# Kernel tuning notes

Measured on AMD Instinct MI355X. Metric: run time of the kernel, lower is better.

## Reference

```python
import jax, jax.numpy as jnp
import numpy as np

N = 50000   # nodes
E = 400000  # edges
R = 35      # num_relations
B = 12      # num_bases
C = 128     # hidden_conv_dim (heads=1)
T = 4       # node types: load, gen, load_gen, ext
HL = 38     # hidden_lin_dim
OUT = 2


def setup_inputs() -> dict:
    key = jax.random.key(0)
    ks = jax.random.split(key, 24)
    s = 0.1  # param scale
    inp = {
        'x': jax.random.normal(ks[0], (N, 2), jnp.float32),
        'edge_index': jax.random.randint(ks[1], (2, E), 0, N, jnp.int32),
        'edge_type': jax.random.randint(ks[2], (E,), 0, R, jnp.int32),
        'edge_attr': jax.random.normal(ks[3], (E, 2), jnp.float32),
        'node_type': jax.random.randint(ks[4], (N,), 0, T, jnp.int32),
        'basis': jax.random.normal(ks[5], (B, 2, C), jnp.float32) * s,
        'att_rel': jax.random.normal(ks[6], (R, B), jnp.float32) * s,
        'q_att': jax.random.normal(ks[7], (C, 1), jnp.float32) * s,
        'k_att': jax.random.normal(ks[8], (C, 1), jnp.float32) * s,
        'e_att': jax.random.normal(ks[9], (C, 1), jnp.float32) * s,
        'lin_edge_W': jax.random.normal(ks[10], (2, C), jnp.float32) * s,
        'conv_bias': jax.random.normal(ks[11], (C,), jnp.float32) * s,
        'lin0_W': jax.random.normal(ks[12], (T, C, HL), jnp.float32) * s,
        'lin0_b': jax.random.normal(ks[13], (T, HL), jnp.float32) * s,
        'lin1_W': jax.random.normal(ks[14], (T, HL, HL), jnp.float32) * s,
        'lin1_b': jax.random.normal(ks[15], (T, HL), jnp.float32) * s,
        'lin2_W': jax.random.normal(ks[16], (T, HL, HL), jnp.float32) * s,
        'lin2_b': jax.random.normal(ks[17], (T, HL), jnp.float32) * s,
        'fin_W': jax.random.normal(ks[18], (T, HL, OUT), jnp.float32) * s,
        'fin_b': jax.random.normal(ks[19], (T, OUT), jnp.float32) * s,
    }
    return inp


def _segment_softmax(alpha, dst, n):
    # PyG softmax: max is detached, eps=1e-16 on the denominator
    amax = jax.lax.stop_gradient(jax.ops.segment_max(alpha, dst, num_segments=n))
    ex = jnp.exp(alpha - amax[dst])
    den = jax.ops.segment_sum(ex, dst, num_segments=n) + 1e-16
    return ex / den[dst]


def _per_type_linear(xv, W, b, t):
    # apply node-type-specific Linear: [N,d] x [T,d,h] -> pick row type
    y = jnp.einsum('nd,tdh->nth', xv, W)              # [N,T,h]
    y = jnp.take_along_axis(y, t[:, None, None], axis=1)[:, 0]
    return y + b[t]


def reference(x, edge_index, edge_type, edge_attr, node_type,
              basis, att_rel, q_att, k_att, e_att, lin_edge_W, conv_bias,
              lin0_W, lin0_b, lin1_W, lin1_b, lin2_W, lin2_b, fin_W, fin_b):
    n = x.shape[0]
    src, dst = edge_index[0], edge_index[1]
    # RGATConv with basis decomposition: per-relation weight [R, in=2, C]
    w = jnp.einsum('rb,bio->rio', att_rel, basis)
    w_e = w[edge_type]                                 # [E,2,C] edge gather
    out_i = jnp.einsum('ei,eic->ec', x[dst], w_e)      # [E,C]
    out_j = jnp.einsum('ei,eic->ec', x[src], w_e)      # [E,C]
    ke = (edge_attr @ lin_edge_W) @ e_att              # [E,1]
    alpha = out_i @ q_att + out_j @ k_att + ke         # additive self-attention
    alpha = jax.nn.leaky_relu(alpha, 0.2)
    alpha = _segment_softmax(alpha, dst, n)            # across-relation segment softmax
    msg = alpha * out_j                                # heads=1 -> [E,C]
    agg = jax.ops.segment_sum(msg, dst, num_segments=n) + conv_bias
    h = jax.nn.leaky_relu(agg, 0.2)                    # forward activation (dropout: eval)
    t = node_type
    h = _per_type_linear(jax.nn.relu(h), lin0_W, lin0_b, t)
    h = _per_type_linear(jax.nn.relu(h), lin1_W, lin1_b, t)
    h = _per_type_linear(jax.nn.relu(h), lin2_W, lin2_b, t)
    out = _per_type_linear(h, fin_W, fin_b, t)         # [N,2]
    # load nodes (type 0): second output passes through abs
    load_out = jnp.concatenate([out[:, :1], jnp.abs(out[:, 1:2])], axis=1)
    return jnp.where((t == 0)[:, None], load_out, out)
```

## Files before the change

kernel.cpp:

```cpp
#include <hip/hip_runtime.h>
#include <math.h>

#define N_NODES 50000
#define N_EDGES 400000
#define R_REL   35
#define B_BASES 12
#define C_DIM   128
#define HL_DIM  38
#define RI2     70
#define NP      50304
#define NB_HIST 196
#define NBUCK   786
#define EPB     2048
#define CAP     704

#define OFF_WT     0
#define OFF_WQ     8960
#define OFF_WK     9030
#define OFF_LE     9100
#define OFF_META   9104
#define OFF_HBLK   9120
#define OFF_BBASE  9904
#define OFF_PERM   10688
#define OFF_INV    60688
#define OFF_ECUR   110992
#define OFF_EREC   111780

#define CH    0
#define ST    3584
#define HH    0
#define Y0T   0
#define W1S   3264
#define W2S   4784
#define Y1T   6304
#define Y2T   0
#define W0Q   8344
#define SM_DINV 9624
#define SM_FW   9688
#define SM_FB   9764
#define LDS_FLOATS 9766

__global__ __launch_bounds__(256) void k_init(const int* __restrict__ node_type,
                                              const float* __restrict__ basis,
                                              const float* __restrict__ att_rel,
                                              float* __restrict__ ws) {
    int b = blockIdx.x, tid = threadIdx.x;
    if (b < NB_HIST) {
        __shared__ int lh[4];
        if (tid < 4) lh[tid] = 0;
        __syncthreads();
        int i = b * 256 + tid;
        if (i < N_NODES) atomicAdd(&lh[node_type[i]], 1);
        __syncthreads();
        if (tid < 4) ((int*)(ws + OFF_HBLK))[b * 4 + tid] = lh[tid];
    } else if (b < NB_HIST + 35) {
        int idx = (b - NB_HIST) * 256 + tid;
        if (idx < RI2 * C_DIM) {
            int c  = idx & (C_DIM - 1);
            int ri = idx >> 7;
            int r = ri >> 1, ii = ri & 1;
            float acc = 0.f;
            #pragma unroll
            for (int bb = 0; bb < B_BASES; ++bb)
                acc += att_rel[r * B_BASES + bb] * basis[(bb * 2 + ii) * C_DIM + c];
            ws[OFF_WT + idx] = acc;
        }
    } else {
        for (int i = tid; i < NBUCK; i += 256) ((int*)(ws + OFF_ECUR))[i] = 0;
    }
}

__global__ __launch_bounds__(256) void k_scanproj(const float* __restrict__ q_att,
                                                  const float* __restrict__ k_att,
                                                  const float* __restrict__ e_att,
                                                  const float* __restrict__ lin_edge_W,
                                                  float* __restrict__ ws) {
    int b = blockIdx.x, tid = threadIdx.x;
    int lane = tid & 63, wv = tid >> 6;
    if (b == 0) {
        __shared__ int lh[NB_HIST * 4];
        __shared__ int basel[4];
        const int* hblk = (const int*)(ws + OFF_HBLK);
        for (int i = tid; i < NB_HIST * 4; i += 256) lh[i] = hblk[i];
        __syncthreads();
        __shared__ int tot[4];
        if (tid < 4) {
            int run = 0;
            for (int bb = 0; bb < NB_HIST; ++bb) {
                int v = lh[bb * 4 + tid];
                lh[bb * 4 + tid] = run;
                run += v;
            }
            tot[tid] = run;
        }
        __syncthreads();
        if (tid == 0) {
            int* meta = (int*)(ws + OFF_META);
            int t0 = tot[0], t1 = tot[1], t2 = tot[2], t3 = tot[3];
            int b1 = ((t0 + 63) >> 6) << 6;
            int b2 = b1 + (((t1 + 63) >> 6) << 6);
            int b3 = b2 + (((t2 + 63) >> 6) << 6);
            meta[0] = t0; meta[1] = t1; meta[2] = t2; meta[3] = t3;
            meta[4] = 0;  meta[5] = b1; meta[6] = b2; meta[7] = b3;
            basel[0] = 0; basel[1] = b1; basel[2] = b2; basel[3] = b3;
        }
        __syncthreads();
        for (int i = tid; i < NB_HIST * 4; i += 256)
            ((int*)(ws + OFF_BBASE))[i] = basel[i & 3] + lh[i];
    } else {
        int u = (b - 1) * 4 + wv;
        if (u < RI2) {
            const float* wr = ws + OFF_WT + u * C_DIM;
            float w1 = wr[lane], w2 = wr[64 + lane];
            float aq = w1 * q_att[lane] + w2 * q_att[64 + lane];
            float ak = w1 * k_att[lane] + w2 * k_att[64 + lane];
            #pragma unroll
            for (int off = 32; off; off >>= 1) {
                aq += __shfl_xor(aq, off, 64);
                ak += __shfl_xor(ak, off, 64);
            }
            if (lane == 0) { ws[OFF_WQ + u] = aq; ws[OFF_WK + u] = ak; }
        } else if (u < 72) {
            int j = u - RI2;
            const float* er = lin_edge_W + j * C_DIM;
            float a = er[lane] * e_att[lane] + er[64 + lane] * e_att[64 + lane];
            #pragma unroll
            for (int off = 32; off; off >>= 1) a += __shfl_xor(a, off, 64);
            if (lane == 0) ws[OFF_LE + j] = a;
        }
    }
}

__global__ __launch_bounds__(256) void k_perm(const int* __restrict__ node_type,
                                              float* __restrict__ ws) {
    __shared__ int wcnt[4][4];
    int tid = threadIdx.x;
    int lane = tid & 63, wv = tid >> 6;
    int n = blockIdx.x * 256 + tid;
    bool active = n < N_NODES;
    int ty = active ? node_type[n] : -1;
    int myrank = 0;
    #pragma unroll
    for (int t = 0; t < 4; ++t) {
        unsigned long long m = __ballot(ty == t);
        if (lane == 0) wcnt[wv][t] = __popcll(m);
        if (ty == t) myrank = __popcll(m & ((1ULL << lane) - 1ULL));
    }
    __syncthreads();
    if (active) {
        int pre = 0;
        for (int w2 = 0; w2 < wv; ++w2) pre += wcnt[w2][ty];
        int p = ((const int*)(ws + OFF_BBASE))[blockIdx.x * 4 + ty] + pre + myrank;
        ((int*)(ws + OFF_PERM))[n] = p;
        ((int*)(ws + OFF_INV))[p] = n;
    }
}

__global__ __launch_bounds__(256) void k_escatter(const float* __restrict__ x,
                                                  const int* __restrict__ edge_index,
                                                  const int* __restrict__ edge_type,
                                                  const float* __restrict__ edge_attr,
                                                  float* __restrict__ ws) {
    __shared__ int hist[NBUCK];
    __shared__ int sbase[NBUCK];
    __shared__ float swq[RI2], swk[RI2], sle[2];
    int tid = threadIdx.x;
    for (int i = tid; i < NBUCK; i += 256) hist[i] = 0;
    if (tid < RI2) { swq[tid] = ws[OFF_WQ + tid]; swk[tid] = ws[OFF_WK + tid]; }
    if (tid < 2) sle[tid] = ws[OFF_LE + tid];
    __syncthreads();

    const int* perm = (const int*)(ws + OFF_PERM);
    int base = blockIdx.x * EPB;
    int   rb[8], rm[8];
    float rex[8], rsx[8], rsy[8];
    #pragma unroll
    for (int k = 0; k < 8; ++k) {
        int e = base + k * 256 + tid;
        rb[k] = -1;
        if (e < N_EDGES) {
            int src = edge_index[e];
            int dst = edge_index[N_EDGES + e];
            int r   = edge_type[e];
            int p   = perm[dst];
            float2 ea = *(const float2*)(edge_attr + 2 * e);
            float2 xs = *(const float2*)(x + 2 * src);
            float2 xd = *(const float2*)(x + 2 * dst);
            float alpha = xd.x * swq[2 * r] + xd.y * swq[2 * r + 1]
                        + xs.x * swk[2 * r] + xs.y * swk[2 * r + 1]
                        + ea.x * sle[0]     + ea.y * sle[1];
            alpha = alpha > 0.f ? alpha : 0.2f * alpha;
            float ex = __expf(alpha);
            rb[k]  = p >> 6;
            rm[k]  = (r << 6) | (p & 63);
            rex[k] = ex;
            rsx[k] = ex * xs.x;
            rsy[k] = ex * xs.y;
            atomicAdd(&hist[rb[k]], 1);
        }
    }
    __syncthreads();
    int* gcur = (int*)(ws + OFF_ECUR);
    for (int i = tid; i < NBUCK; i += 256) {
        int c = hist[i];
        sbase[i] = (c > 0) ? atomicAdd(&gcur[i], c) : 0;
    }
    __syncthreads();
    float4* rec = (float4*)(ws + OFF_EREC);
    #pragma unroll
    for (int k = 0; k < 8; ++k) {
        if (rb[k] >= 0) {
            int slot = atomicAdd(&sbase[rb[k]], 1);
            rec[(size_t)rb[k] * CAP + slot] =
                make_float4(__int_as_float(rm[k]), rex[k], rsx[k], rsy[k]);
        }
    }
}

__global__ __launch_bounds__(256) void k_node(
        const float* __restrict__ ws, const float* __restrict__ conv_bias,
        const float* __restrict__ lin0_W, const float* __restrict__ lin0_b,
        const float* __restrict__ lin1_W, const float* __restrict__ lin1_b,
        const float* __restrict__ lin2_W, const float* __restrict__ lin2_b,
        const float* __restrict__ fin_W,  const float* __restrict__ fin_b,
        float* __restrict__ out) {
    __shared__ float L[LDS_FLOATS];
    int tid  = threadIdx.x;
    int lane = tid & 63;
    int wv   = tid >> 6;
    int p0   = blockIdx.x * 64;

    const int* meta = (const int*)(ws + OFF_META);
    int b1 = meta[5], b2 = meta[6], b3 = meta[7];
    int t  = (p0 >= b1) + (p0 >= b2) + (p0 >= b3);
    int bp = meta[4 + t];
    int cnt = meta[t];

    for (int i = tid; i < RI2 * 68; i += 256) L[ST + i] = 0.f;
    if (tid < 64) L[SM_DINV + tid] = 0.f;
    if (tid >= 64 && tid < 142) {
        int i = tid - 64;
        if (i < 76) L[SM_FW + i] = fin_W[t * 76 + i];
        else        L[SM_FB + i - 76] = fin_b[t * 2 + i - 76];
    }
    const float* wT_g = ws + OFF_WT;
    for (int i4 = tid; i4 < 448; i4 += 256) {
        float4 v = ((const float4*)wT_g)[i4];
        *(float4*)&L[CH + i4 * 4] = v;
    }
    __syncthreads();

    {
        int ecnt = ((const int*)(ws + OFF_ECUR))[blockIdx.x];
        const float4* rec = (const float4*)(ws + OFF_EREC) + (size_t)blockIdx.x * CAP;
        for (int i = tid; i < ecnt; i += 256) {
            float4 v = rec[i];
            int m = __float_as_int(v.x);
            int n = m & 63, r = m >> 6;
            atomicAdd(&L[ST + (2 * r) * 68 + n],     v.z);
            atomicAdd(&L[ST + (2 * r + 1) * 68 + n], v.w);
            atomicAdd(&L[SM_DINV + n],               v.y);
        }
    }
    __syncthreads();
    if (tid < 64) L[SM_DINV + tid] = 1.0f / (L[SM_DINV + tid] + 1e-16f);

    int ng = lane & 15, cg_ = lane >> 4;
    int c0 = wv * 32 + cg_ * 8;
    float acc[32];
    #pragma unroll
    for (int i = 0; i < 32; ++i) acc[i] = 0.f;
    int cur = 0;
    for (int q = 0; q < 5; ++q) {
        float4 pf0, pf1;
        if (q < 4) {
            const float4* src = (const float4*)(wT_g + (q + 1) * 1792);
            pf0 = src[tid];
            if (tid < 192) pf1 = src[tid + 256];
        }
        const float* wb = &L[CH + cur * 1792];
        #pragma unroll
        for (int kk = 0; kk < 14; ++kk) {
            float4 a4 = *(const float4*)&L[ST + (q * 14 + kk) * 68 + ng * 4];
            float4 wa = *(const float4*)&wb[kk * 128 + c0];
            float4 wc = *(const float4*)&wb[kk * 128 + c0 + 4];
            float a_[4] = {a4.x, a4.y, a4.z, a4.w};
            float w_[8] = {wa.x, wa.y, wa.z, wa.w, wc.x, wc.y, wc.z, wc.w};
            #pragma unroll
            for (int ni = 0; ni < 4; ++ni)
                #pragma unroll
                for (int ci = 0; ci < 8; ++ci)
                    acc[ni * 8 + ci] += a_[ni] * w_[ci];
        }
        if (q < 4) {
            float* dstb = &L[CH + (cur ^ 1) * 1792];
            *(float4*)&dstb[tid * 4] = pf0;
            if (tid < 192) *(float4*)&dstb[(tid + 256) * 4] = pf1;
        }
        cur ^= 1;
        __syncthreads();
    }

    {
        float4 dv = *(const float4*)&L[SM_DINV + ng * 4];
        float d_[4] = {dv.x, dv.y, dv.z, dv.w};
        #pragma unroll
        for (int ci = 0; ci < 8; ++ci) {
            float cb = conv_bias[c0 + ci];
            float4 hv;
            float h0 = acc[0 * 8 + ci] * d_[0] + cb;
            float h1 = acc[1 * 8 + ci] * d_[1] + cb;
            float h2 = acc[2 * 8 + ci] * d_[2] + cb;
            float h3 = acc[3 * 8 + ci] * d_[3] + cb;
            hv.x = h0 > 0.f ? h0 : 0.f;
            hv.y = h1 > 0.f ? h1 : 0.f;
            hv.z = h2 > 0.f ? h2 : 0.f;
            hv.w = h3 > 0.f ? h3 : 0.f;
            *(float4*)&L[HH + (c0 + ci) * 64 + ng * 4] = hv;
        }
    }
    __syncthreads();

    const float* W0g = lin0_W + t * C_DIM * HL_DIM;
    int jg = lane >> 4;
    int j0 = wv * 16 + jg * 4;
    float acc2[16];
    #pragma unroll
    for (int i = 0; i < 16; ++i) acc2[i] = 0.f;
    for (int q = 0; q < 4; ++q) {
        for (int i = tid; i < 1216; i += 256) {
            int cc = i / 38, j = i - cc * 38;
            L[W0Q + cc * 40 + j] = W0g[q * 1216 + i];
        }
        __syncthreads();
        if (wv < 3) {
            #pragma unroll 4
            for (int kk = 0; kk < 32; ++kk) {
                int c = q * 32 + kk;
                float4 a4 = *(const float4*)&L[HH + c * 64 + ng * 4];
                float4 w4 = *(const float4*)&L[W0Q + kk * 40 + j0];
                float a_[4] = {a4.x, a4.y, a4.z, a4.w};
                float w_[4] = {w4.x, w4.y, w4.z, w4.w};
                #pragma unroll
                for (int ni = 0; ni < 4; ++ni)
                    #pragma unroll
                    for (int ji = 0; ji < 4; ++ji)
                        acc2[ni * 4 + ji] += a_[ni] * w_[ji];
            }
        }
        __syncthreads();
    }
    if (wv < 3) {
        #pragma unroll
        for (int ji = 0; ji < 4; ++ji) {
            int j = j0 + ji;
            float b = (j < HL_DIM) ? lin0_b[t * HL_DIM + j] : 0.f;
            float4 yv;
            float y0 = acc2[0 * 4 + ji] + b;
            float y1 = acc2[1 * 4 + ji] + b;
            float y2 = acc2[2 * 4 + ji] + b;
            float y3 = acc2[3 * 4 + ji] + b;
            yv.x = y0 > 0.f ? y0 : 0.f;
            yv.y = y1 > 0.f ? y1 : 0.f;
            yv.z = y2 > 0.f ? y2 : 0.f;
            yv.w = y3 > 0.f ? y3 : 0.f;
            *(float4*)&L[Y0T + j * 68 + ng * 4] = yv;
        }
    }
    {
        const float* W1g = lin1_W + t * HL_DIM * HL_DIM;
        const float* W2g = lin2_W + t * HL_DIM * HL_DIM;
        for (int i = tid; i < 1444; i += 256) {
            int cc = i / 38, j = i - cc * 38;
            L[W1S + cc * 40 + j] = W1g[i];
            L[W2S + cc * 40 + j] = W2g[i];
        }
    }
    __syncthreads();

    float acc3[16];
    #pragma unroll
    for (int i = 0; i < 16; ++i) acc3[i] = 0.f;
    if (wv < 3) {
        #pragma unroll 2
        for (int kk = 0; kk < HL_DIM; ++kk) {
            float4 a4 = *(const float4*)&L[Y0T + kk * 68 + ng * 4];
            float4 w4 = *(const float4*)&L[W1S + kk * 40 + j0];
            float a_[4] = {a4.x, a4.y, a4.z, a4.w};
            float w_[4] = {w4.x, w4.y, w4.z, w4.w};
            #pragma unroll
            for (int ni = 0; ni < 4; ++ni)
                #pragma unroll
                for (int ji = 0; ji < 4; ++ji)
                    acc3[ni * 4 + ji] += a_[ni] * w_[ji];
        }
        #pragma unroll
        for (int ji = 0; ji < 4; ++ji) {
            int j = j0 + ji;
            float b = (j < HL_DIM) ? lin1_b[t * HL_DIM + j] : 0.f;
            float4 yv;
            float y0 = acc3[0 * 4 + ji] + b;
            float y1 = acc3[1 * 4 + ji] + b;
            float y2 = acc3[2 * 4 + ji] + b;
            float y3 = acc3[3 * 4 + ji] + b;
            yv.x = y0 > 0.f ? y0 : 0.f;
            yv.y = y1 > 0.f ? y1 : 0.f;
            yv.z = y2 > 0.f ? y2 : 0.f;
            yv.w = y3 > 0.f ? y3 : 0.f;
            *(float4*)&L[Y1T + j * 68 + ng * 4] = yv;
        }
    }
    __syncthreads();

    if (wv < 3) {
        float acc4[16];
        #pragma unroll
        for (int i = 0; i < 16; ++i) acc4[i] = 0.f;
        #pragma unroll 2
        for (int kk = 0; kk < HL_DIM; ++kk) {
            float4 a4 = *(const float4*)&L[Y1T + kk * 68 + ng * 4];
            float4 w4 = *(const float4*)&L[W2S + kk * 40 + j0];
            float a_[4] = {a4.x, a4.y, a4.z, a4.w};
            float w_[4] = {w4.x, w4.y, w4.z, w4.w};
            #pragma unroll
            for (int ni = 0; ni < 4; ++ni)
                #pragma unroll
                for (int ji = 0; ji < 4; ++ji)
                    acc4[ni * 4 + ji] += a_[ni] * w_[ji];
        }
        #pragma unroll
        for (int ji = 0; ji < 4; ++ji) {
            int j = j0 + ji;
            float b = (j < HL_DIM) ? lin2_b[t * HL_DIM + j] : 0.f;
            float4 yv;
            yv.x = acc4[0 * 4 + ji] + b;
            yv.y = acc4[1 * 4 + ji] + b;
            yv.z = acc4[2 * 4 + ji] + b;
            yv.w = acc4[3 * 4 + ji] + b;
            *(float4*)&L[Y2T + j * 68 + ng * 4] = yv;
        }
    }
    __syncthreads();

    if (tid < 64) {
        int p = p0 + tid;
        bool valid = (p - bp) < cnt;
        float o0 = L[SM_FB], o1 = L[SM_FB + 1];
        for (int jj = 0; jj < HL_DIM; ++jj) {
            float v = L[Y2T + jj * 68 + tid];
            float2 f = *(const float2*)&L[SM_FW + jj * 2];
            o0 += v * f.x;
            o1 += v * f.y;
        }
        if (t == 0) o1 = fabsf(o1);
        if (valid) {
            int orig = ((const int*)(ws + OFF_INV))[p];
            ((float2*)out)[orig] = make_float2(o0, o1);
        }
    }
}

extern "C" void kernel_launch(void* const* d_in, const int* in_sizes, int n_in,
                              void* d_out, int out_size, void* d_ws, size_t ws_size,
                              hipStream_t stream) {
    const float* x          = (const float*)d_in[0];
    const int*   edge_index = (const int*)  d_in[1];
    const int*   edge_type  = (const int*)  d_in[2];
    const float* edge_attr  = (const float*)d_in[3];
    const int*   node_type  = (const int*)  d_in[4];
    const float* basis      = (const float*)d_in[5];
    const float* att_rel    = (const float*)d_in[6];
    const float* q_att      = (const float*)d_in[7];
    const float* k_att      = (const float*)d_in[8];
    const float* e_att      = (const float*)d_in[9];
    const float* lin_edge_W = (const float*)d_in[10];
    const float* conv_bias  = (const float*)d_in[11];
    const float* lin0_W     = (const float*)d_in[12];
    const float* lin0_b     = (const float*)d_in[13];
    const float* lin1_W     = (const float*)d_in[14];
    const float* lin1_b     = (const float*)d_in[15];
    const float* lin2_W     = (const float*)d_in[16];
    const float* lin2_b     = (const float*)d_in[17];
    const float* fin_W      = (const float*)d_in[18];
    const float* fin_b      = (const float*)d_in[19];

    float* ws  = (float*)d_ws;
    float* out = (float*)d_out;

    k_init    <<<NB_HIST + 35 + 1, 256, 0, stream>>>(node_type, basis, att_rel, ws);
    k_scanproj<<<19, 256, 0, stream>>>(q_att, k_att, e_att, lin_edge_W, ws);
    k_perm    <<<NB_HIST, 256, 0, stream>>>(node_type, ws);
    k_escatter<<<NB_HIST, 256, 0, stream>>>(x, edge_index, edge_type, edge_attr, ws);
    k_node    <<<NBUCK, 256, 0, stream>>>(ws, conv_bias,
                                          lin0_W, lin0_b, lin1_W, lin1_b,
                                          lin2_W, lin2_b, fin_W, fin_b, out);
}
```

Before: 177.7 us.

## Fold scan/projection kernel into init and perm kernels to drop a launch

Removes the k_scanproj kernel. The q/k/e attention projections move into extra k_init blocks, which recompute the basis-combined weights directly instead of reading them back from the workspace. Each k_perm block now redundantly scans the per-block type histogram to find its own prefix and the type bases. This removes one kernel launch and its dependency gap, at the cost of redundant serial scan work in every perm block.

```diff
diff --git a/kernel.cpp b/kernel.cpp
--- a/kernel.cpp
+++ b/kernel.cpp
@@ -20,7 +20,6 @@
 #define OFF_LE     9100
 #define OFF_META   9104
 #define OFF_HBLK   9120
-#define OFF_BBASE  9904
 #define OFF_PERM   10688
 #define OFF_INV    60688
 #define OFF_ECUR   110992
@@ -43,6 +42,10 @@
 __global__ __launch_bounds__(256) void k_init(const int* __restrict__ node_type,
                                               const float* __restrict__ basis,
                                               const float* __restrict__ att_rel,
+                                              const float* __restrict__ q_att,
+                                              const float* __restrict__ k_att,
+                                              const float* __restrict__ e_att,
+                                              const float* __restrict__ lin_edge_W,
                                               float* __restrict__ ws) {
     int b = blockIdx.x, tid = threadIdx.x;
     if (b < NB_HIST) {
@@ -65,77 +68,72 @@
                 acc += att_rel[r * B_BASES + bb] * basis[(bb * 2 + ii) * C_DIM + c];
             ws[OFF_WT + idx] = acc;
         }
+    } else if (b == NB_HIST + 35) {
+        for (int i = tid; i < NBUCK; i += 256) ((int*)(ws + OFF_ECUR))[i] = 0;
     } else {
-        for (int i = tid; i < NBUCK; i += 256) ((int*)(ws + OFF_ECUR))[i] = 0;
-    }
-}
-
-__global__ __launch_bounds__(256) void k_scanproj(const float* __restrict__ q_att,
-                                                  const float* __restrict__ k_att,
-                                                  const float* __restrict__ e_att,
-                                                  const float* __restrict__ lin_edge_W,
-                                                  float* __restrict__ ws) {
-    int b = blockIdx.x, tid = threadIdx.x;
-    int lane = tid & 63, wv = tid >> 6;
-    if (b == 0) {
-        __shared__ int lh[NB_HIST * 4];
-        __shared__ int basel[4];
-        const int* hblk = (const int*)(ws + OFF_HBLK);
-        for (int i = tid; i < NB_HIST * 4; i += 256) lh[i] = hblk[i];
-        __syncthreads();
-        __shared__ int tot[4];
-        if (tid < 4) {
-            int run = 0;
-            for (int bb = 0; bb < NB_HIST; ++bb) {
-                int v = lh[bb * 4 + tid];
-                lh[bb * 4 + tid] = run;
-                run += v;
+        int lane = tid & 63, wv = tid >> 6;
+        int u = (b - (NB_HIST + 36)) * 4 + wv;
+        if (u < 2 * RI2) {
+            int ri = (u < RI2) ? u : (u - RI2);
+            int r = ri >> 1, ii = ri & 1;
+            const float* av = att_rel + r * B_BASES;
+            const float* bs = basis + ii * C_DIM;
+            float w1 = 0.f, w2 = 0.f;
+            #pragma unroll
+            for (int bb = 0; bb < B_BASES; ++bb) {
+                float a = av[bb];
+                w1 += a * bs[bb * 2 * C_DIM + lane];
+                w2 += a * bs[bb * 2 * C_DIM + 64 + lane];
             }
-            tot[tid] = run;
-        }
-        __syncthreads();
-        if (tid == 0) {
-            int* meta = (int*)(ws + OFF_META);
-            int t0 = tot[0], t1 = tot[1], t2 = tot[2], t3 = tot[3];
-            int b1 = ((t0 + 63) >> 6) << 6;
-            int b2 = b1 + (((t1 + 63) >> 6) << 6);
-            int b3 = b2 + (((t2 + 63) >> 6) << 6);
-            meta[0] = t0; meta[1] = t1; meta[2] = t2; meta[3] = t3;
-            meta[4] = 0;  meta[5] = b1; meta[6] = b2; meta[7] = b3;
-            basel[0] = 0; basel[1] = b1; basel[2] = b2; basel[3] = b3;
-        }
-        __syncthreads();
-        for (int i = tid; i < NB_HIST * 4; i += 256)
-            ((int*)(ws + OFF_BBASE))[i] = basel[i & 3] + lh[i];
-    } else {
-        int u = (b - 1) * 4 + wv;
-        if (u < RI2) {
-            const float* wr = ws + OFF_WT + u * C_DIM;
-            float w1 = wr[lane], w2 = wr[64 + lane];
-            float aq = w1 * q_att[lane] + w2 * q_att[64 + lane];
-            float ak = w1 * k_att[lane] + w2 * k_att[64 + lane];
-            #pragma unroll
-            for (int off = 32; off; off >>= 1) {
-                aq += __shfl_xor(aq, off, 64);
-                ak += __shfl_xor(ak, off, 64);
-            }
-            if (lane == 0) { ws[OFF_WQ + u] = aq; ws[OFF_WK + u] = ak; }
-        } else if (u < 72) {
-            int j = u - RI2;
+            const float* qk = (u < RI2) ? q_att : k_att;
+            float s = w1 * qk[lane] + w2 * qk[64 + lane];
+            #pragma unroll
+            for (int off = 32; off; off >>= 1) s += __shfl_xor(s, off, 64);
+            if (lane == 0) ws[((u < RI2) ? OFF_WQ : OFF_WK) + ri] = s;
+        } else if (u < 2 * RI2 + 2) {
+            int j = u - 2 * RI2;
             const float* er = lin_edge_W + j * C_DIM;
-            float a = er[lane] * e_att[lane] + er[64 + lane] * e_att[64 + lane];
-            #pragma unroll
-            for (int off = 32; off; off >>= 1) a += __shfl_xor(a, off, 64);
-            if (lane == 0) ws[OFF_LE + j] = a;
+            float s = er[lane] * e_att[lane] + er[64 + lane] * e_att[64 + lane];
+            #pragma unroll
+            for (int off = 32; off; off >>= 1) s += __shfl_xor(s, off, 64);
+            if (lane == 0) ws[OFF_LE + j] = s;
         }
     }
 }
 
 __global__ __launch_bounds__(256) void k_perm(const int* __restrict__ node_type,
                                               float* __restrict__ ws) {
+    __shared__ int lh[NB_HIST * 4];
+    __shared__ int pre[4], tot[4], basel[4];
     __shared__ int wcnt[4][4];
     int tid = threadIdx.x;
     int lane = tid & 63, wv = tid >> 6;
+    const int* hblk = (const int*)(ws + OFF_HBLK);
+    for (int i = tid; i < NB_HIST * 4; i += 256) lh[i] = hblk[i];
+    __syncthreads();
+    if (tid < 4) {
+        int run = 0, mypre = 0;
+        for (int bb = 0; bb < NB_HIST; ++bb) {
+            if (bb == (int)blockIdx.x) mypre = run;
+            run += lh[bb * 4 + tid];
+        }
+        pre[tid] = mypre;
+        tot[tid] = run;
+    }
+    __syncthreads();
+    if (tid == 0) {
+        int t0 = tot[0], t1 = tot[1], t2 = tot[2];
+        int b1 = ((t0 + 63) >> 6) << 6;
+        int b2 = b1 + (((t1 + 63) >> 6) << 6);
+        int b3 = b2 + (((t2 + 63) >> 6) << 6);
+        basel[0] = 0; basel[1] = b1; basel[2] = b2; basel[3] = b3;
+        if (blockIdx.x == 0) {
+            int* meta = (int*)(ws + OFF_META);
+            meta[0] = t0; meta[1] = t1; meta[2] = t2; meta[3] = tot[3];
+            meta[4] = 0;  meta[5] = b1; meta[6] = b2; meta[7] = b3;
+        }
+    }
+    __syncthreads();
     int n = blockIdx.x * 256 + tid;
     bool active = n < N_NODES;
     int ty = active ? node_type[n] : -1;
@@ -148,9 +146,9 @@
     }
     __syncthreads();
     if (active) {
-        int pre = 0;
-        for (int w2 = 0; w2 < wv; ++w2) pre += wcnt[w2][ty];
-        int p = ((const int*)(ws + OFF_BBASE))[blockIdx.x * 4 + ty] + pre + myrank;
+        int prew = 0;
+        for (int w2 = 0; w2 < wv; ++w2) prew += wcnt[w2][ty];
+        int p = basel[ty] + pre[ty] + prew + myrank;
         ((int*)(ws + OFF_PERM))[n] = p;
         ((int*)(ws + OFF_INV))[p] = n;
     }
@@ -487,8 +485,8 @@
     float* ws  = (float*)d_ws;
     float* out = (float*)d_out;
 
-    k_init    <<<NB_HIST + 35 + 1, 256, 0, stream>>>(node_type, basis, att_rel, ws);
-    k_scanproj<<<19, 256, 0, stream>>>(q_att, k_att, e_att, lin_edge_W, ws);
+    k_init    <<<NB_HIST + 35 + 1 + 36, 256, 0, stream>>>(node_type, basis, att_rel,
+                                                          q_att, k_att, e_att, lin_edge_W, ws);
     k_perm    <<<NB_HIST, 256, 0, stream>>>(node_type, ws);
     k_escatter<<<NB_HIST, 256, 0, stream>>>(x, edge_index, edge_type, edge_attr, ws);
     k_node    <<<NBUCK, 256, 0, stream>>>(ws, conv_bias,
```

After: 176.1 us. No clear change (-0.9%).
